# Performance work log

Measured on AMD Instinct MI355X. Metric: run time of the kernel, lower is better.

The kernel has to match this reference:

```python
import jax, jax.numpy as jnp
import numpy as np

HIDDEN = 5120
NUM_HEADS = 32
Q_LORA = 1536
KV_LORA = 512
NOPE = 128
ROPE = 64
V_DIM = 128
QK = NOPE + ROPE  # 192
T = 2048
ROPE_BASE = 10000.0
EPS = 1e-6


def setup_inputs() -> dict:
    key = jax.random.key(0)
    ks = jax.random.split(key, 8)
    s = 0.02
    return {
        "positions": jnp.arange(T, dtype=jnp.int64 if jax.config.jax_enable_x64 else jnp.int32),
        "hidden_states": jax.random.normal(ks[0], (T, HIDDEN), dtype=jnp.float32),
        "w_q_a": jax.random.normal(ks[1], (HIDDEN, Q_LORA), dtype=jnp.float32) * s,
        "q_a_norm": jnp.ones((Q_LORA,), dtype=jnp.float32),
        "w_q_b": jax.random.normal(ks[2], (Q_LORA, NUM_HEADS * QK), dtype=jnp.float32) * s,
        "w_kv_a": jax.random.normal(ks[3], (HIDDEN, KV_LORA + ROPE), dtype=jnp.float32) * s,
        "kv_a_norm": jnp.ones((KV_LORA,), dtype=jnp.float32),
        "w_kv_b": jax.random.normal(ks[4], (KV_LORA, NUM_HEADS * (NOPE + V_DIM)), dtype=jnp.float32) * s,
        "w_o": jax.random.normal(ks[5], (NUM_HEADS * V_DIM, HIDDEN), dtype=jnp.float32) * s,
    }


def _rmsnorm(x, w):
    var = jnp.mean(x * x, axis=-1, keepdims=True)
    return x * jax.lax.rsqrt(var + EPS) * w


def _rope_interleaved(x, positions):
    # x: [T, H, ROPE]; interleaved (GPT-J style) rotation, pairs (x[2i], x[2i+1])
    half = ROPE // 2
    inv_freq = 1.0 / (ROPE_BASE ** (jnp.arange(half, dtype=jnp.float32) * 2.0 / ROPE))
    angles = positions.astype(jnp.float32)[:, None] * inv_freq[None, :]  # [T, half]
    cos = jnp.cos(angles)[:, None, :]  # [T, 1, half]
    sin = jnp.sin(angles)[:, None, :]
    x1 = x[..., 0::2]
    x2 = x[..., 1::2]
    r1 = x1 * cos - x2 * sin
    r2 = x1 * sin + x2 * cos
    return jnp.stack([r1, r2], axis=-1).reshape(x.shape)


def reference(positions, hidden_states, w_q_a, q_a_norm, w_q_b, w_kv_a, kv_a_norm, w_kv_b, w_o):
    # Q path: down-proj -> RMSNorm -> up-proj -> split(nope, rope)
    q_c = _rmsnorm(hidden_states @ w_q_a, q_a_norm)
    q = (q_c @ w_q_b).reshape(T, NUM_HEADS, QK)
    q_nope, q_rope = q[:, :, :NOPE], q[:, :, NOPE:]

    # KV path: joint down-proj -> split(compressed, k_rope) -> RMSNorm -> up-proj
    kv_a = hidden_states @ w_kv_a
    compressed = _rmsnorm(kv_a[:, :KV_LORA], kv_a_norm)
    k_rope_raw = kv_a[:, KV_LORA:].reshape(T, 1, ROPE)
    kv = (compressed @ w_kv_b).reshape(T, NUM_HEADS, NOPE + V_DIM)
    k_nope, v = kv[:, :, :NOPE], kv[:, :, NOPE:]

    # RoPE on rope slices only (interleaved style since rope_interleave=True)
    q_rope = _rope_interleaved(q_rope, positions)
    k_rope = _rope_interleaved(k_rope_raw, positions)
    k_rope = jnp.broadcast_to(k_rope, (T, NUM_HEADS, ROPE))

    q_full = jnp.concatenate([q_nope, q_rope], axis=-1)  # [T, H, QK]
    k_full = jnp.concatenate([k_nope, k_rope], axis=-1)  # [T, H, QK]

    # Causal attention (RadixAttention prefill), scaling = qk_head_dim**-0.5.
    # v is zero-padded to QK in the source and sliced back after; using v
    # directly is mathematically identical.
    scale = QK ** (-0.5)
    scores = jnp.einsum("thd,shd->hts", q_full, k_full) * scale  # [H, T, T]
    causal = positions[:, None] >= positions[None, :]
    scores = jnp.where(causal[None, :, :], scores, jnp.float32(-1e30))
    probs = jax.nn.softmax(scores, axis=-1)
    attn = jnp.einsum("hts,shd->thd", probs, v)  # [T, H, V_DIM]

    out = attn.reshape(T, NUM_HEADS * V_DIM) @ w_o  # [T, HIDDEN]
    return out
```

## Files before the change

### kernel.cpp

```cpp
#include <hip/hip_runtime.h>

typedef unsigned short u16;
typedef unsigned int   u32;
typedef __bf16 bf16x8 __attribute__((ext_vector_type(8)));
typedef float  f32x4  __attribute__((ext_vector_type(4)));
typedef u16    u16x4  __attribute__((ext_vector_type(4)));
typedef u16    u16x8  __attribute__((ext_vector_type(8)));

__device__ __forceinline__ u16 f2bf(float f) {
  u32 u = __float_as_uint(f);
  u32 r = u + 0x7fffu + ((u >> 16) & 1u);
  return (u16)(r >> 16);
}

__device__ __forceinline__ void gl16(const void* g, void* l) {
  __builtin_amdgcn_global_load_lds((__attribute__((address_space(1))) void*)(g),
                                   (__attribute__((address_space(3))) void*)(l),
                                   16, 0, 0);
}

#define WAITVM4  asm volatile("s_waitcnt vmcnt(4)" ::: "memory")
#define WAITVM0  asm volatile("s_waitcnt vmcnt(0)" ::: "memory")
#define WAITLG0  asm volatile("s_waitcnt lgkmcnt(0)" ::: "memory")
#define BAR()    asm volatile("s_barrier" ::: "memory")
#define SCHEDB() __builtin_amdgcn_sched_barrier(0)

__device__ __forceinline__ void tr_tile(const float* __restrict__ W, u16* __restrict__ Wt,
                                        int K, int N, int NT, int idx, float (*tile)[65]) {
  const int tid = threadIdx.x;
  const int nt = idx % NT, kt = idx / NT;
  const int n0 = nt * 64, k0 = kt * 32;
  {
    const int r = tid >> 3, c8 = (tid & 7) << 3;
    const float* src = W + (size_t)(k0 + r) * N + n0 + c8;
    float4 a = *(const float4*)src;
    float4 b = *(const float4*)(src + 4);
    tile[r][c8 + 0] = a.x; tile[r][c8 + 1] = a.y; tile[r][c8 + 2] = a.z; tile[r][c8 + 3] = a.w;
    tile[r][c8 + 4] = b.x; tile[r][c8 + 5] = b.y; tile[r][c8 + 6] = b.z; tile[r][c8 + 7] = b.w;
  }
  __syncthreads();
  const int n = tid >> 2, kg = (tid & 3) << 3;
  u16x8 o;
  #pragma unroll
  for (int j = 0; j < 8; ++j) o[j] = f2bf(tile[kg + j][n]);
  *(u16x8*)(Wt + (size_t)(n0 + n) * K + k0 + kg) = o;
}

__global__ __launch_bounds__(256) void prep_w(const float* __restrict__ hidden, u16* __restrict__ hs_bf,
                                              const float* __restrict__ wqa,  u16* __restrict__ wqa_t,
                                              const float* __restrict__ wkva, u16* __restrict__ wkva_t,
                                              const float* __restrict__ wqb,  u16* __restrict__ wqb_t,
                                              const float* __restrict__ wkvb, u16* __restrict__ wkvb_t,
                                              const float* __restrict__ wo,   u16* __restrict__ wo_t) {
  __shared__ float tile[32][65];
  const int b = blockIdx.x, tid = threadIdx.x;
  if (b < 640) {
    const float4* xin = (const float4*)hidden;
    #pragma unroll
    for (int j = 0; j < 8; ++j) {
      int u = b * 2048 + j * 256 + tid;
      float4 a = xin[u * 2], c = xin[u * 2 + 1];
      u16x8 o;
      o[0] = f2bf(a.x); o[1] = f2bf(a.y); o[2] = f2bf(a.z); o[3] = f2bf(a.w);
      o[4] = f2bf(c.x); o[5] = f2bf(c.y); o[6] = f2bf(c.z); o[7] = f2bf(c.w);
      *(u16x8*)(hs_bf + (size_t)u * 8) = o;
    }
  } else if (b < 4480) {
    tr_tile(wqa, wqa_t, 5120, 1536, 24, b - 640, tile);
  } else if (b < 5920) {
    tr_tile(wkva, wkva_t, 5120, 576, 9, b - 4480, tile);
  } else if (b < 10528) {
    tr_tile(wqb, wqb_t, 1536, 6144, 96, b - 5920, tile);
  } else if (b < 12576) {
    tr_tile(wkvb, wkvb_t, 512, 8192, 128, b - 10528, tile);
  } else if (b < 22816) {
    tr_tile(wo, wo_t, 4096, 5120, 80, b - 12576, tile);
  } else {
    int off = (b - 22816) * 4096 + tid * 16;
    u16x8 z = {};
    *(u16x8*)((char*)wkva_t + (size_t)576 * 5120 * 2 + off) = z;
  }
}

__global__ __launch_bounds__(256) void gemm_a(const u16* __restrict__ A,
                                              const u16* __restrict__ Bt,
                                              float* __restrict__ C,
                                              int M, int N, int K, int nkt) {
  __shared__ u16 As[128 * 64];
  __shared__ u16 Bs[128 * 64];
  const int tid = threadIdx.x;
  const int lane = tid & 63, w = tid >> 6;
  const int n0 = blockIdx.x << 7, m0 = blockIdx.y << 7;
  const int kt0 = blockIdx.z * nkt;
  float* Cs = C + (size_t)blockIdx.z * M * N;
  const int wr = w >> 1, wc = w & 1;
  const int lr = lane & 15, lg = lane >> 4;
  f32x4 acc[4][4] = {};
  const char* Ab = (const char*)A;
  const char* Bb = (const char*)Bt;
  const int stageOff = (w << 10) + (lane << 4);
  for (int kt = 0; kt < nkt; ++kt) {
    __syncthreads();
    const size_t kb = (size_t)(kt0 + kt) << 7;
    #pragma unroll
    for (int o = 0; o < 16384; o += 4096) {
      int ofs = stageOff + o;
      int row = ofs >> 7;
      int cb  = ofs & 127;
      gl16(Ab + (size_t)(m0 + row) * K * 2 + kb + cb, (char*)As + ofs);
      gl16(Bb + (size_t)(n0 + row) * K * 2 + kb + cb, (char*)Bs + ofs);
    }
    __syncthreads();
    bf16x8 a[4][2], b[4][2];
    #pragma unroll
    for (int m = 0; m < 4; ++m)
      #pragma unroll
      for (int kf = 0; kf < 2; ++kf)
        a[m][kf] = *(const bf16x8*)(As + ((wr * 64 + m * 16 + lr) * 64 + kf * 32 + lg * 8));
    #pragma unroll
    for (int n = 0; n < 4; ++n)
      #pragma unroll
      for (int kf = 0; kf < 2; ++kf)
        b[n][kf] = *(const bf16x8*)(Bs + ((wc * 64 + n * 16 + lr) * 64 + kf * 32 + lg * 8));
    #pragma unroll
    for (int kf = 0; kf < 2; ++kf)
      #pragma unroll
      for (int m = 0; m < 4; ++m)
        #pragma unroll
        for (int n = 0; n < 4; ++n)
          acc[m][n] = __builtin_amdgcn_mfma_f32_16x16x32_bf16(a[m][kf], b[n][kf], acc[m][n], 0, 0, 0);
  }
  #pragma unroll
  for (int m = 0; m < 4; ++m) {
    const int row0 = m0 + wr * 64 + m * 16 + lg * 4;
    #pragma unroll
    for (int n = 0; n < 4; ++n) {
      const int col = n0 + wc * 64 + n * 16 + lr;
      #pragma unroll
      for (int r = 0; r < 4; ++r)
        Cs[(size_t)(row0 + r) * N + col] = acc[m][n][r];
    }
  }
}

template<int EPI>
__device__ __forceinline__ void gemm8_body(char* lds,
                                           const u16* __restrict__ A,
                                           const u16* __restrict__ Bt,
                                           int N, int K, int wg, int nwg, int nbx,
                                           const int* __restrict__ pos,
                                           u16* __restrict__ q_all,
                                           u16* __restrict__ k_all,
                                           u16* __restrict__ v_big,
                                           float* __restrict__ Cf) {
  const int nkt = K >> 6;
  const int tid = threadIdx.x;
  const int lane = tid & 63, wid = tid >> 6;
  const int wr = wid >> 2, wc = wid & 3;
  const int lr = lane & 15, lg = lane >> 4;

  const int swz = ((nwg & 7) == 0) ? ((wg & 7) * (nwg >> 3) + (wg >> 3)) : wg;
  const int bx = swz % nbx, by = swz / nbx;
  const int m0 = by << 8, n0 = bx << 8;

  const size_t rs = (size_t)K << 1;
  const char* Ab = (const char*)A;
  const char* Bb = (const char*)Bt;

  const int sofs = tid << 4;
  const int srow = sofs >> 7;
  const int scol = ((((sofs >> 4) & 7) ^ (srow & 7)) << 4);

  const int axor = lr & 7;
  const int sx0 = (lg ^ axor) << 4;
  const int sx1 = ((4 | lg) ^ axor) << 4;
  const int bcolbase = (wc & 1) << 13;

  f32x4 acc[8][4] = {};

#define ASL(p,h) ((((p) << 1) | (h)) << 14)
#define BSL(p,h) (65536 + ((((p) << 1) | (h)) << 14))
#define STAGE_HALF(gb, grow0, kt, slot)                                              \
  { const char* _s = (gb) + (size_t)(grow0) * rs + ((size_t)(kt) << 7) + scol;       \
    gl16(_s, lds + (slot) + sofs);                                                   \
    gl16(_s + (rs << 6), lds + (slot) + sofs + 8192); }

  STAGE_HALF(Ab, m0 + srow,       0, ASL(0,0));
  STAGE_HALF(Ab, m0 + 128 + srow, 0, ASL(0,1));
  STAGE_HALF(Bb, n0 + srow,       0, BSL(0,0));
  STAGE_HALF(Bb, n0 + 128 + srow, 0, BSL(0,1));
  if (nkt > 1) {
    STAGE_HALF(Bb, n0 + srow,       1, BSL(1,0));
    STAGE_HALF(Bb, n0 + 128 + srow, 1, BSL(1,1));
    WAITVM4;
  } else {
    WAITVM0;
  }
  BAR();

  for (int b = 0; b < nkt; ++b) {
    const int p = b & 1;
    const int abase = ASL(p, wr);
    const int bbase = BSL(p, (wc >> 1)) + bcolbase;
    bf16x8 aR[4][2], bR[4][2];

    #pragma unroll
    for (int m = 0; m < 4; ++m) {
      aR[m][0] = *(const bf16x8*)(lds + abase + (m * 16 + lr) * 128 + sx0);
      aR[m][1] = *(const bf16x8*)(lds + abase + (m * 16 + lr) * 128 + sx1);
    }
    #pragma unroll
    for (int n = 0; n < 2; ++n) {
      bR[n][0] = *(const bf16x8*)(lds + bbase + (n * 16 + lr) * 128 + sx0);
      bR[n][1] = *(const bf16x8*)(lds + bbase + (n * 16 + lr) * 128 + sx1);
    }
    if (b + 1 < nkt) { STAGE_HALF(Ab, m0 + srow, b + 1, ASL((b + 1) & 1, 0)); }
    BAR(); WAITLG0; SCHEDB();
    __builtin_amdgcn_s_setprio(1);
    #pragma unroll
    for (int kf = 0; kf < 2; ++kf)
      #pragma unroll
      for (int m = 0; m < 4; ++m)
        #pragma unroll
        for (int n = 0; n < 2; ++n)
          acc[m][n] = __builtin_amdgcn_mfma_f32_16x16x32_bf16(aR[m][kf], bR[n][kf], acc[m][n], 0, 0, 0);
    __builtin_amdgcn_s_setprio(0); SCHEDB();
    BAR();

    #pragma unroll
    for (int n = 2; n < 4; ++n) {
      bR[n][0] = *(const bf16x8*)(lds + bbase + (n * 16 + lr) * 128 + sx0);
      bR[n][1] = *(const bf16x8*)(lds + bbase + (n * 16 + lr) * 128 + sx1);
    }
    if (b + 1 < nkt) { STAGE_HALF(Ab, m0 + 128 + srow, b + 1, ASL((b + 1) & 1, 1)); }
    BAR(); WAITLG0; SCHEDB();
    __builtin_amdgcn_s_setprio(1);
    #pragma unroll
    for (int kf = 0; kf < 2; ++kf)
      #pragma unroll
      for (int m = 0; m < 4; ++m)
        #pragma unroll
        for (int n = 2; n < 4; ++n)
          acc[m][n] = __builtin_amdgcn_mfma_f32_16x16x32_bf16(aR[m][kf], bR[n][kf], acc[m][n], 0, 0, 0);
    __builtin_amdgcn_s_setprio(0); SCHEDB();
    BAR();

    #pragma unroll
    for (int m = 0; m < 4; ++m) {
      aR[m][0] = *(const bf16x8*)(lds + abase + ((m + 4) * 16 + lr) * 128 + sx0);
      aR[m][1] = *(const bf16x8*)(lds + abase + ((m + 4) * 16 + lr) * 128 + sx1);
    }
    if (b + 2 < nkt) { STAGE_HALF(Bb, n0 + srow, b + 2, BSL(p, 0)); }
    BAR(); WAITLG0; SCHEDB();
    __builtin_amdgcn_s_setprio(1);
    #pragma unroll
    for (int kf = 0; kf < 2; ++kf)
      #pragma unroll
      for (int m = 0; m < 4; ++m)
        #pragma unroll
        for (int n = 0; n < 2; ++n)
          acc[m + 4][n] = __builtin_amdgcn_mfma_f32_16x16x32_bf16(aR[m][kf], bR[n][kf], acc[m + 4][n], 0, 0, 0);
    __builtin_amdgcn_s_setprio(0); SCHEDB();
    BAR();

    if (b + 2 < nkt) { STAGE_HALF(Bb, n0 + 128 + srow, b + 2, BSL(p, 1)); }
    BAR(); SCHEDB();
    __builtin_amdgcn_s_setprio(1);
    #pragma unroll
    for (int kf = 0; kf < 2; ++kf)
      #pragma unroll
      for (int m = 0; m < 4; ++m)
        #pragma unroll
        for (int n = 2; n < 4; ++n)
          acc[m + 4][n] = __builtin_amdgcn_mfma_f32_16x16x32_bf16(aR[m][kf], bR[n][kf], acc[m + 4][n], 0, 0, 0);
    __builtin_amdgcn_s_setprio(0); SCHEDB();
    if (b + 2 < nkt) { WAITVM4; } else { WAITVM0; }
    BAR();
  }

  if (EPI == 0) {
    #pragma unroll
    for (int m = 0; m < 8; ++m) {
      const int row0 = m0 + wr * 128 + m * 16 + lg * 4;
      #pragma unroll
      for (int n = 0; n < 4; ++n) {
        const int col = n0 + wc * 64 + n * 16 + lr;
        #pragma unroll
        for (int r = 0; r < 4; ++r)
          Cf[(size_t)(row0 + r) * N + col] = acc[m][n][r];
      }
    }
  } else if (EPI == 1) {
    int hh[4], dd[4]; float inv[4]; bool rope[4];
    #pragma unroll
    for (int n = 0; n < 4; ++n) {
      int col = n0 + wc * 64 + n * 16 + lr;
      hh[n] = col / 192;
      dd[n] = col - hh[n] * 192;
      rope[n] = (dd[n] >= 128);
      int i = (dd[n] - 128) >> 1;
      inv[n] = rope[n] ? exp2f(-(float)i * 0.41524101186092f) : 0.f;
    }
    const bool odd = (lr & 1);
    #pragma unroll
    for (int m = 0; m < 8; ++m) {
      const int row0 = m0 + wr * 128 + m * 16 + lg * 4;
      #pragma unroll
      for (int r = 0; r < 4; ++r) {
        const int row = row0 + r;
        const float pv = (float)pos[row];
        #pragma unroll
        for (int n = 0; n < 4; ++n) {
          float v = acc[m][n][r];
          float o = __shfl_xor(v, 1, 64);
          if (rope[n]) {
            float s, c;
            __sincosf(pv * inv[n], &s, &c);
            v = odd ? (o * s + v * c) : (v * c - o * s);
          }
          q_all[((size_t)hh[n] * 2048 + row) * 192 + dd[n]] = f2bf(v);
        }
      }
    }
  } else {
    #pragma unroll
    for (int m = 0; m < 8; ++m) {
      const int row0 = m0 + wr * 128 + m * 16 + lg * 4;
      #pragma unroll
      for (int r = 0; r < 4; ++r) {
        const int row = row0 + r;
        #pragma unroll
        for (int n = 0; n < 4; ++n) {
          const int col = n0 + wc * 64 + n * 16 + lr;
          const int h = col >> 8, dd = col & 255;
          u16 bv = f2bf(acc[m][n][r]);
          if (dd < 128) k_all[((size_t)h * 2048 + row) * 200 + dd] = bv;
          else          v_big[(size_t)row * 4096 + h * 128 + (dd - 128)] = bv;
        }
      }
    }
  }
#undef ASL
#undef BSL
#undef STAGE_HALF
}

__global__ __launch_bounds__(512, 2) void gemm_fused_b(const u16* __restrict__ A1,
                                                       const u16* __restrict__ B1,
                                                       const u16* __restrict__ A2,
                                                       const u16* __restrict__ B2,
                                                       const int* __restrict__ pos,
                                                       u16* __restrict__ q_all,
                                                       u16* __restrict__ k_all,
                                                       u16* __restrict__ v_big) {
  __shared__ char lds[131072];
  if (blockIdx.x < 192)
    gemm8_body<1>(lds, A1, B1, 6144, 1536, blockIdx.x, 192, 24, pos, q_all, nullptr, nullptr, nullptr);
  else
    gemm8_body<2>(lds, A2, B2, 8192, 512, blockIdx.x - 192, 256, 32, pos, nullptr, k_all, v_big, nullptr);
}

__global__ __launch_bounds__(512, 2) void gemm_out_k(const u16* __restrict__ A,
                                                     const u16* __restrict__ Bt,
                                                     float* __restrict__ C) {
  __shared__ char lds[131072];
  gemm8_body<0>(lds, A, Bt, 5120, 4096, blockIdx.x, 160, 20, nullptr, nullptr, nullptr, nullptr, C);
}

#define SLAB ((size_t)2048 * 2176)
__global__ __launch_bounds__(256) void norm_q_kernel(const float* __restrict__ x,
                                                     const float* __restrict__ w,
                                                     u16* __restrict__ y) {
  const int row = blockIdx.x, tid = threadIdx.x;
  const float* xr = x + (size_t)row * 2176;
  float v[6]; float ss = 0.f;
  #pragma unroll
  for (int i = 0; i < 6; ++i) {
    size_t o = tid + i * 256;
    v[i] = xr[o] + xr[o + SLAB] + xr[o + 2 * SLAB] + xr[o + 3 * SLAB];
    ss += v[i] * v[i];
  }
  __shared__ float sm[4];
  #pragma unroll
  for (int o = 32; o > 0; o >>= 1) ss += __shfl_down(ss, o, 64);
  if ((tid & 63) == 0) sm[tid >> 6] = ss;
  __syncthreads();
  float tot = sm[0] + sm[1] + sm[2] + sm[3];
  float rs = rsqrtf(tot * (1.f / 1536.f) + 1e-6f);
  #pragma unroll
  for (int i = 0; i < 6; ++i)
    y[(size_t)row * 1536 + tid + i * 256] = f2bf(v[i] * rs * w[tid + i * 256]);
}

__global__ __launch_bounds__(256) void norm_kv_kernel(const float* __restrict__ kva,
                                                      const float* __restrict__ w,
                                                      const int* __restrict__ pos,
                                                      u16* __restrict__ comp,
                                                      u16* __restrict__ krope) {
  const int row = blockIdx.x, tid = threadIdx.x;
  const float* xr = kva + (size_t)row * 2176 + 1536;
  float v0 = xr[tid] + xr[tid + SLAB] + xr[tid + 2 * SLAB] + xr[tid + 3 * SLAB];
  size_t o1 = tid + 256;
  float v1 = xr[o1] + xr[o1 + SLAB] + xr[o1 + 2 * SLAB] + xr[o1 + 3 * SLAB];
  float ss = v0 * v0 + v1 * v1;
  __shared__ float sm[4];
  #pragma unroll
  for (int o = 32; o > 0; o >>= 1) ss += __shfl_down(ss, o, 64);
  if ((tid & 63) == 0) sm[tid >> 6] = ss;
  __syncthreads();
  float tot = sm[0] + sm[1] + sm[2] + sm[3];
  float rs = rsqrtf(tot * (1.f / 512.f) + 1e-6f);
  comp[(size_t)row * 512 + tid]       = f2bf(v0 * rs * w[tid]);
  comp[(size_t)row * 512 + tid + 256] = f2bf(v1 * rs * w[tid + 256]);
  if (tid < 32) {
    float p = (float)pos[row];
    float inv = powf(10000.0f, -(float)(2 * tid) * (1.0f / 64.0f));
    float ang = p * inv;
    float c = cosf(ang), s = sinf(ang);
    size_t e1 = 512 + 2 * tid, e2 = e1 + 1;
    float x1 = xr[e1] + xr[e1 + SLAB] + xr[e1 + 2 * SLAB] + xr[e1 + 3 * SLAB];
    float x2 = xr[e2] + xr[e2 + SLAB] + xr[e2 + 2 * SLAB] + xr[e2 + 3 * SLAB];
    krope[(size_t)row * 64 + 2 * tid]     = f2bf(x1 * c - x2 * s);
    krope[(size_t)row * 64 + 2 * tid + 1] = f2bf(x1 * s + x2 * c);
  }
}

__global__ __launch_bounds__(256) void krope_bcast(const u16* __restrict__ krope,
                                                   u16* __restrict__ k_all) {
  const int s = blockIdx.x, tid = threadIdx.x;
  const int h = tid >> 3, j8 = (tid & 7) << 3;
  *(u16x8*)&k_all[((size_t)h * 2048 + s) * 200 + 128 + j8] =
      *(const u16x8*)&krope[(size_t)s * 64 + j8];
}

__global__ __launch_bounds__(256) void v_transpose(const u16* __restrict__ v_big,
                                                   u16* __restrict__ v_t) {
  const int h = blockIdx.x & 31, st = blockIdx.x >> 5, tid = threadIdx.x;
  const int s0 = st * 64;
  __shared__ u16 vs[64][128];
  for (int idx = tid; idx < 4096; idx += 256) {
    int s = idx >> 6, d2 = idx & 63;
    *(u32*)&vs[s][d2 * 2] = *(const u32*)&v_big[(size_t)(s0 + s) * 4096 + h * 128 + d2 * 2];
  }
  __syncthreads();
  const int d = tid >> 1, sh = (tid & 1) * 32;
  u16 tmp[32];
  #pragma unroll
  for (int i = 0; i < 32; ++i) tmp[i] = vs[sh + i][d];
  #pragma unroll
  for (int b = 0; b < 4; ++b) {
    u16x8 o;
    #pragma unroll
    for (int j = 0; j < 8; ++j) o[j] = tmp[b * 8 + j];
    *(u16x8*)(v_t + ((size_t)h * 128 + d) * 2048 + s0 + sh + b * 8) = o;
  }
}

#define SCL2 0.10412706f
#define THR2 11.5f
__global__ __launch_bounds__(512, 2) void attn_fwd(const u16* __restrict__ q_all,
                                                   const u16* __restrict__ k_all,
                                                   const u16* __restrict__ v_t,
                                                   u16* __restrict__ attnb) {
  __shared__ __align__(16) char lds[106496];
  const int tid = threadIdx.x;
  const int lane = tid & 63, wid = tid >> 6;
  const int lr = lane & 15, lg = lane >> 4;
  const int h = blockIdx.x & 31, bq = blockIdx.x >> 5;

  const char* kh = (const char*)(k_all + (size_t)h * 2048 * 200);
  const char* vh = (const char*)(v_t + (size_t)h * 128 * 2048);
  char* Pw = lds + 88064 + wid * 2304;

  const int nCalls = (wid < 3) ? 6 : 5;
  const char* gp[6]; int cofs[6]; int isK[6];
  #pragma unroll
  for (int ii = 0; ii < 6; ++ii) {
    int i = wid + (ii << 3);
    if (i < 43) {
      int c = (i << 6) + lane;
      cofs[ii] = c << 4;
      if (c < 1600) { gp[ii] = kh + ((size_t)c << 4); isK[ii] = 1; }
      else {
        int cv = c - 1600;
        int row = cv / 9, sub = cv - row * 9;
        gp[ii] = vh + ((size_t)row << 12) + ((sub < 8) ? (sub << 4) : 0);
        isK[ii] = 0;
      }
    } else { gp[ii] = kh; cofs[ii] = 0; isK[ii] = 1; }
  }

#define STAGE(s0_, bOff_)                                                       \
  { int _sk = (s0_) * 400, _sv = (s0_) * 2;                                     \
    _Pragma("unroll")                                                           \
    for (int ii = 0; ii < 6; ++ii)                                              \
      if (ii < nCalls)                                                          \
        gl16(gp[ii] + (isK[ii] ? _sk : _sv), lds + (bOff_) + cofs[ii]); }

#define WAITSTAGE                                                               \
  { if (wid < 3) { asm volatile("s_waitcnt vmcnt(6)" ::: "memory"); }           \
    else        { asm volatile("s_waitcnt vmcnt(5)" ::: "memory"); } }

  const int kRd = lr * 400 + lg * 16;
  const int vRd = lr * 144 + lg * 16;
  const int pRd = lr * 144 + lg * 16;
  const int pWr = lr * 144 + lg * 8;

  #pragma unroll
  for (int half = 0; half < 2; ++half) {
    const int qt = half ? (15 - bq) : bq;
    const int qb0 = qt << 7;
    const int nt = 2 * qt + 2;
    const int qlane = qb0 + wid * 16 + lr;
    const int qwmin = qb0 + wid * 16;

    bf16x8 qf[6];
    const u16* qptr = q_all + ((size_t)h * 2048 + qlane) * 192 + lg * 8;
    #pragma unroll
    for (int kf = 0; kf < 6; ++kf) qf[kf] = *(const bf16x8*)(qptr + kf * 32);

    f32x4 O[8] = {};
    float m = -1e30f, l = 0.f;

    STAGE(0, 0);
    for (int st = 0; st < nt; ++st) {
      const int s0 = st << 6;
      const int bOff = (st & 1) * 44032;
      if (st + 1 < nt) {
        STAGE((st + 1) << 6, ((st + 1) & 1) * 44032);
        WAITSTAGE;
      } else {
        WAITVM0;
      }
      BAR();

      const bool active = (s0 <= qwmin + 15);
      if (active) {
        const char* Kb = lds + bOff;
        const char* Vb = lds + bOff + 25600;

        f32x4 S[4];
        #pragma unroll
        for (int sb = 0; sb < 4; ++sb) {
          f32x4 a = {};
          #pragma unroll
          for (int kf = 0; kf < 6; ++kf) {
            bf16x8 kfr = *(const bf16x8*)(Kb + kRd + sb * 6400 + kf * 64);
            a = __builtin_amdgcn_mfma_f32_16x16x32_bf16(kfr, qf[kf], a, 0, 0, 0);
          }
          S[sb] = a;
        }

        if (s0 + 63 > qwmin) {
          const int kb0 = s0 + lg * 4;
          #pragma unroll
          for (int sb = 0; sb < 4; ++sb)
            #pragma unroll
            for (int r = 0; r < 4; ++r) {
              int k = kb0 + sb * 16 + r;
              S[sb][r] = (k > qlane) ? -1e30f : S[sb][r] * SCL2;
            }
        } else {
          #pragma unroll
          for (int sb = 0; sb < 4; ++sb)
            #pragma unroll
            for (int r = 0; r < 4; ++r) S[sb][r] *= SCL2;
        }

        float mx = S[0][0];
        #pragma unroll
        for (int sb = 0; sb < 4; ++sb)
          #pragma unroll
          for (int r = 0; r < 4; ++r) mx = fmaxf(mx, S[sb][r]);
        mx = fmaxf(mx, __shfl_xor(mx, 16, 64));
        mx = fmaxf(mx, __shfl_xor(mx, 32, 64));

        const bool skip = __all(mx <= m + THR2);
        float alpha = 1.f;
        if (!skip) { float mn = fmaxf(m, mx); alpha = exp2f(m - mn); m = mn; }

        float ps = 0.f;
        #pragma unroll
        for (int sb = 0; sb < 4; ++sb)
          #pragma unroll
          for (int r = 0; r < 4; ++r) {
            float pv = exp2f(S[sb][r] - m);
            S[sb][r] = pv;
            ps += pv;
          }
        ps += __shfl_xor(ps, 16, 64);
        ps += __shfl_xor(ps, 32, 64);
        l = l * alpha + ps;

        if (!skip) {
          float aO[4];
          #pragma unroll
          for (int r = 0; r < 4; ++r) aO[r] = __shfl(alpha, lg * 4 + r, 64);
          #pragma unroll
          for (int nb = 0; nb < 8; ++nb)
            #pragma unroll
            for (int r = 0; r < 4; ++r) O[nb][r] *= aO[r];
        }

        #pragma unroll
        for (int sb = 0; sb < 4; ++sb) {
          u32 p01, p23;
          asm("v_cvt_pk_bf16_f32 %0, %1, %2" : "=v"(p01) : "v"(S[sb][0]), "v"(S[sb][1]));
          asm("v_cvt_pk_bf16_f32 %0, %1, %2" : "=v"(p23) : "v"(S[sb][2]), "v"(S[sb][3]));
          *(uint2*)(Pw + pWr + sb * 32) = make_uint2(p01, p23);
        }

        #pragma unroll
        for (int k2 = 0; k2 < 2; ++k2) {
          bf16x8 pa = *(const bf16x8*)(Pw + pRd + k2 * 64);
          #pragma unroll
          for (int nb = 0; nb < 8; ++nb) {
            bf16x8 vf = *(const bf16x8*)(Vb + vRd + nb * 2304 + k2 * 64);
            O[nb] = __builtin_amdgcn_mfma_f32_16x16x32_bf16(pa, vf, O[nb], 0, 0, 0);
          }
        }
      }
      BAR();
    }

    float rv[4];
    #pragma unroll
    for (int r = 0; r < 4; ++r) rv[r] = 1.f / __shfl(l, lg * 4 + r, 64);
    #pragma unroll
    for (int nb = 0; nb < 8; ++nb) {
      const int col = h * 128 + nb * 16 + lr;
      #pragma unroll
      for (int r = 0; r < 4; ++r)
        attnb[(size_t)(qb0 + wid * 16 + lg * 4 + r) * 4096 + col] = f2bf(O[nb][r] * rv[r]);
    }
  }
#undef STAGE
#undef WAITSTAGE
}

extern "C" void kernel_launch(void* const* d_in, const int* in_sizes, int n_in,
                              void* d_out, int out_size, void* d_ws, size_t ws_size,
                              hipStream_t stream) {
  const int*   positions = (const int*)d_in[0];
  const float* hidden    = (const float*)d_in[1];
  const float* w_q_a     = (const float*)d_in[2];
  const float* q_a_norm  = (const float*)d_in[3];
  const float* w_q_b     = (const float*)d_in[4];
  const float* w_kv_a    = (const float*)d_in[5];
  const float* kv_a_norm = (const float*)d_in[6];
  const float* w_kv_b    = (const float*)d_in[7];
  const float* w_o       = (const float*)d_in[8];
  float* out = (float*)d_out;
  char*  ws  = (char*)d_ws;

  u16* hs_bf  = (u16*)(ws + 0);
  u16* attnb  = (u16*)(ws + 0);
  u16* wqa_t  = (u16*)(ws + 20971520);
  u16* wkva_t = (u16*)(ws + 36700160);
  u16* q_c_n  = (u16*)(ws + 20971520);
  u16* comp   = (u16*)(ws + 27262976);
  u16* krope  = (u16*)(ws + 29360128);
  u16* wqb_t  = (u16*)(ws + 43253760);
  u16* wkvb_t = (u16*)(ws + 62128128);
  u16* wo_t   = (u16*)(ws + 70516736);
  float* slabs = (float*)(ws + 112459776);
  u16* q_all  = (u16*)(ws + 112459776);
  u16* k_all  = (u16*)(ws + 137625600);
  u16* v_big  = (u16*)(ws + 183762944);
  u16* v_t    = (u16*)(ws + 200540160);

  prep_w<<<22976, 256, 0, stream>>>(hidden, hs_bf, w_q_a, wqa_t, w_kv_a, wkva_t,
                                    w_q_b, wqb_t, w_kv_b, wkvb_t, w_o, wo_t);

  gemm_a<<<dim3(17, 16, 4), 256, 0, stream>>>(hs_bf, wqa_t, slabs, 2048, 2176, 5120, 20);

  norm_q_kernel<<<2048, 256, 0, stream>>>(slabs, q_a_norm, q_c_n);
  norm_kv_kernel<<<2048, 256, 0, stream>>>(slabs, kv_a_norm, positions, comp, krope);
  krope_bcast<<<2048, 256, 0, stream>>>(krope, k_all);

  gemm_fused_b<<<448, 512, 0, stream>>>(q_c_n, wqb_t, comp, wkvb_t, positions,
                                        q_all, k_all, v_big);

  v_transpose<<<1024, 256, 0, stream>>>(v_big, v_t);

  attn_fwd<<<256, 512, 0, stream>>>(q_all, k_all, v_t, attnb);

  gemm_out_k<<<160, 512, 0, stream>>>(attnb, wo_t, out);
}
```

Before: 453.4 us.

## Replace down-projection GEMM with 256x256 tiled split-K kernel reusing gemm8 body

```diff
diff --git a/kernel.cpp b/kernel.cpp
--- a/kernel.cpp
+++ b/kernel.cpp
@@ -47,8 +47,8 @@
 }
 
 __global__ __launch_bounds__(256) void prep_w(const float* __restrict__ hidden, u16* __restrict__ hs_bf,
-                                              const float* __restrict__ wqa,  u16* __restrict__ wqa_t,
-                                              const float* __restrict__ wkva, u16* __restrict__ wkva_t,
+                                              const float* __restrict__ wqa,
+                                              const float* __restrict__ wkva, u16* __restrict__ wab_t,
                                               const float* __restrict__ wqb,  u16* __restrict__ wqb_t,
                                               const float* __restrict__ wkvb, u16* __restrict__ wkvb_t,
                                               const float* __restrict__ wo,   u16* __restrict__ wo_t) {
@@ -66,9 +66,9 @@
       *(u16x8*)(hs_bf + (size_t)u * 8) = o;
     }
   } else if (b < 4480) {
-    tr_tile(wqa, wqa_t, 5120, 1536, 24, b - 640, tile);
+    tr_tile(wqa, wab_t, 5120, 1536, 24, b - 640, tile);
   } else if (b < 5920) {
-    tr_tile(wkva, wkva_t, 5120, 576, 9, b - 4480, tile);
+    tr_tile(wkva, wab_t + (size_t)1536 * 5120, 5120, 576, 9, b - 4480, tile);
   } else if (b < 10528) {
     tr_tile(wqb, wqb_t, 1536, 6144, 96, b - 5920, tile);
   } else if (b < 12576) {
@@ -76,70 +76,9 @@
   } else if (b < 22816) {
     tr_tile(wo, wo_t, 4096, 5120, 80, b - 12576, tile);
   } else {
-    int off = (b - 22816) * 4096 + tid * 16;
+    size_t off = (size_t)(b - 22816) * 4096 + tid * 16;
     u16x8 z = {};
-    *(u16x8*)((char*)wkva_t + (size_t)576 * 5120 * 2 + off) = z;
-  }
-}
-
-__global__ __launch_bounds__(256) void gemm_a(const u16* __restrict__ A,
-                                              const u16* __restrict__ Bt,
-                                              float* __restrict__ C,
-                                              int M, int N, int K, int nkt) {
-  __shared__ u16 As[128 * 64];
-  __shared__ u16 Bs[128 * 64];
-  const int tid = threadIdx.x;
-  const int lane = tid & 63, w = tid >> 6;
-  const int n0 = blockIdx.x << 7, m0 = blockIdx.y << 7;
-  const int kt0 = blockIdx.z * nkt;
-  float* Cs = C + (size_t)blockIdx.z * M * N;
-  const int wr = w >> 1, wc = w & 1;
-  const int lr = lane & 15, lg = lane >> 4;
-  f32x4 acc[4][4] = {};
-  const char* Ab = (const char*)A;
-  const char* Bb = (const char*)Bt;
-  const int stageOff = (w << 10) + (lane << 4);
-  for (int kt = 0; kt < nkt; ++kt) {
-    __syncthreads();
-    const size_t kb = (size_t)(kt0 + kt) << 7;
-    #pragma unroll
-    for (int o = 0; o < 16384; o += 4096) {
-      int ofs = stageOff + o;
-      int row = ofs >> 7;
-      int cb  = ofs & 127;
-      gl16(Ab + (size_t)(m0 + row) * K * 2 + kb + cb, (char*)As + ofs);
-      gl16(Bb + (size_t)(n0 + row) * K * 2 + kb + cb, (char*)Bs + ofs);
-    }
-    __syncthreads();
-    bf16x8 a[4][2], b[4][2];
-    #pragma unroll
-    for (int m = 0; m < 4; ++m)
-      #pragma unroll
-      for (int kf = 0; kf < 2; ++kf)
-        a[m][kf] = *(const bf16x8*)(As + ((wr * 64 + m * 16 + lr) * 64 + kf * 32 + lg * 8));
-    #pragma unroll
-    for (int n = 0; n < 4; ++n)
-      #pragma unroll
-      for (int kf = 0; kf < 2; ++kf)
-        b[n][kf] = *(const bf16x8*)(Bs + ((wc * 64 + n * 16 + lr) * 64 + kf * 32 + lg * 8));
-    #pragma unroll
-    for (int kf = 0; kf < 2; ++kf)
-      #pragma unroll
-      for (int m = 0; m < 4; ++m)
-        #pragma unroll
-        for (int n = 0; n < 4; ++n)
-          acc[m][n] = __builtin_amdgcn_mfma_f32_16x16x32_bf16(a[m][kf], b[n][kf], acc[m][n], 0, 0, 0);
-  }
-  #pragma unroll
-  for (int m = 0; m < 4; ++m) {
-    const int row0 = m0 + wr * 64 + m * 16 + lg * 4;
-    #pragma unroll
-    for (int n = 0; n < 4; ++n) {
-      const int col = n0 + wc * 64 + n * 16 + lr;
-      #pragma unroll
-      for (int r = 0; r < 4; ++r)
-        Cs[(size_t)(row0 + r) * N + col] = acc[m][n][r];
-    }
+    *(u16x8*)((char*)wab_t + (size_t)2112 * 5120 * 2 + off) = z;
   }
 }
 
@@ -148,12 +87,12 @@
                                            const u16* __restrict__ A,
                                            const u16* __restrict__ Bt,
                                            int N, int K, int wg, int nwg, int nbx,
+                                           int nkt, int kt0,
                                            const int* __restrict__ pos,
                                            u16* __restrict__ q_all,
                                            u16* __restrict__ k_all,
                                            u16* __restrict__ v_big,
                                            float* __restrict__ Cf) {
-  const int nkt = K >> 6;
   const int tid = threadIdx.x;
   const int lane = tid & 63, wid = tid >> 6;
   const int wr = wid >> 2, wc = wid & 3;
@@ -181,7 +120,7 @@
 #define ASL(p,h) ((((p) << 1) | (h)) << 14)
 #define BSL(p,h) (65536 + ((((p) << 1) | (h)) << 14))
 #define STAGE_HALF(gb, grow0, kt, slot)                                              \
-  { const char* _s = (gb) + (size_t)(grow0) * rs + ((size_t)(kt) << 7) + scol;       \
+  { const char* _s = (gb) + (size_t)(grow0) * rs + ((size_t)((kt) + kt0) << 7) + scol; \
     gl16(_s, lds + (slot) + sofs);                                                   \
     gl16(_s + (rs << 6), lds + (slot) + sofs + 8192); }
 
@@ -345,6 +284,19 @@
 #undef STAGE_HALF
 }
 
+#define SLAB2 ((size_t)2048 * 2304)
+__global__ __launch_bounds__(512, 2) void gemm_a8(const u16* __restrict__ A,
+                                                  const u16* __restrict__ Bt,
+                                                  float* __restrict__ C) {
+  __shared__ char lds[131072];
+  const int z = blockIdx.x / 72;
+  const int wg = blockIdx.x - z * 72;
+  const int nkt = (z == 2) ? 26 : 27;
+  const int kt0 = z * 27;
+  gemm8_body<0>(lds, A, Bt, 2304, 5120, wg, 72, 9, nkt, kt0,
+                nullptr, nullptr, nullptr, nullptr, C + (size_t)z * SLAB2);
+}
+
 __global__ __launch_bounds__(512, 2) void gemm_fused_b(const u16* __restrict__ A1,
                                                        const u16* __restrict__ B1,
                                                        const u16* __restrict__ A2,
@@ -355,29 +307,29 @@
                                                        u16* __restrict__ v_big) {
   __shared__ char lds[131072];
   if (blockIdx.x < 192)
-    gemm8_body<1>(lds, A1, B1, 6144, 1536, blockIdx.x, 192, 24, pos, q_all, nullptr, nullptr, nullptr);
+    gemm8_body<1>(lds, A1, B1, 6144, 1536, blockIdx.x, 192, 24, 24, 0, pos, q_all, nullptr, nullptr, nullptr);
   else
-    gemm8_body<2>(lds, A2, B2, 8192, 512, blockIdx.x - 192, 256, 32, pos, nullptr, k_all, v_big, nullptr);
+    gemm8_body<2>(lds, A2, B2, 8192, 512, blockIdx.x - 192, 256, 32, 8, 0, pos, nullptr, k_all, v_big, nullptr);
 }
 
 __global__ __launch_bounds__(512, 2) void gemm_out_k(const u16* __restrict__ A,
                                                      const u16* __restrict__ Bt,
                                                      float* __restrict__ C) {
   __shared__ char lds[131072];
-  gemm8_body<0>(lds, A, Bt, 5120, 4096, blockIdx.x, 160, 20, nullptr, nullptr, nullptr, nullptr, C);
-}
-
-#define SLAB ((size_t)2048 * 2176)
+  gemm8_body<0>(lds, A, Bt, 5120, 4096, blockIdx.x, 160, 20, 64, 0,
+                nullptr, nullptr, nullptr, nullptr, C);
+}
+
 __global__ __launch_bounds__(256) void norm_q_kernel(const float* __restrict__ x,
                                                      const float* __restrict__ w,
                                                      u16* __restrict__ y) {
   const int row = blockIdx.x, tid = threadIdx.x;
-  const float* xr = x + (size_t)row * 2176;
+  const float* xr = x + (size_t)row * 2304;
   float v[6]; float ss = 0.f;
   #pragma unroll
   for (int i = 0; i < 6; ++i) {
     size_t o = tid + i * 256;
-    v[i] = xr[o] + xr[o + SLAB] + xr[o + 2 * SLAB] + xr[o + 3 * SLAB];
+    v[i] = xr[o] + xr[o + SLAB2] + xr[o + 2 * SLAB2];
     ss += v[i] * v[i];
   }
   __shared__ float sm[4];
@@ -398,10 +350,10 @@
                                                       u16* __restrict__ comp,
                                                       u16* __restrict__ krope) {
   const int row = blockIdx.x, tid = threadIdx.x;
-  const float* xr = kva + (size_t)row * 2176 + 1536;
-  float v0 = xr[tid] + xr[tid + SLAB] + xr[tid + 2 * SLAB] + xr[tid + 3 * SLAB];
+  const float* xr = kva + (size_t)row * 2304 + 1536;
+  float v0 = xr[tid] + xr[tid + SLAB2] + xr[tid + 2 * SLAB2];
   size_t o1 = tid + 256;
-  float v1 = xr[o1] + xr[o1 + SLAB] + xr[o1 + 2 * SLAB] + xr[o1 + 3 * SLAB];
+  float v1 = xr[o1] + xr[o1 + SLAB2] + xr[o1 + 2 * SLAB2];
   float ss = v0 * v0 + v1 * v1;
   __shared__ float sm[4];
   #pragma unroll
@@ -418,8 +370,8 @@
     float ang = p * inv;
     float c = cosf(ang), s = sinf(ang);
     size_t e1 = 512 + 2 * tid, e2 = e1 + 1;
-    float x1 = xr[e1] + xr[e1 + SLAB] + xr[e1 + 2 * SLAB] + xr[e1 + 3 * SLAB];
-    float x2 = xr[e2] + xr[e2 + SLAB] + xr[e2 + 2 * SLAB] + xr[e2 + 3 * SLAB];
+    float x1 = xr[e1] + xr[e1 + SLAB2] + xr[e1 + 2 * SLAB2];
+    float x2 = xr[e2] + xr[e2 + SLAB2] + xr[e2 + 2 * SLAB2];
     krope[(size_t)row * 64 + 2 * tid]     = f2bf(x1 * c - x2 * s);
     krope[(size_t)row * 64 + 2 * tid + 1] = f2bf(x1 * s + x2 * c);
   }
@@ -655,24 +607,23 @@
 
   u16* hs_bf  = (u16*)(ws + 0);
   u16* attnb  = (u16*)(ws + 0);
-  u16* wqa_t  = (u16*)(ws + 20971520);
-  u16* wkva_t = (u16*)(ws + 36700160);
+  u16* wab_t  = (u16*)(ws + 20971520);
   u16* q_c_n  = (u16*)(ws + 20971520);
   u16* comp   = (u16*)(ws + 27262976);
   u16* krope  = (u16*)(ws + 29360128);
-  u16* wqb_t  = (u16*)(ws + 43253760);
-  u16* wkvb_t = (u16*)(ws + 62128128);
-  u16* wo_t   = (u16*)(ws + 70516736);
-  float* slabs = (float*)(ws + 112459776);
-  u16* q_all  = (u16*)(ws + 112459776);
-  u16* k_all  = (u16*)(ws + 137625600);
-  u16* v_big  = (u16*)(ws + 183762944);
-  u16* v_t    = (u16*)(ws + 200540160);
-
-  prep_w<<<22976, 256, 0, stream>>>(hidden, hs_bf, w_q_a, wqa_t, w_kv_a, wkva_t,
+  u16* wqb_t  = (u16*)(ws + 44564480);
+  u16* wkvb_t = (u16*)(ws + 63438848);
+  u16* wo_t   = (u16*)(ws + 71827456);
+  float* slabs = (float*)(ws + 113770496);
+  u16* q_all  = (u16*)(ws + 113770496);
+  u16* k_all  = (u16*)(ws + 138936320);
+  u16* v_big  = (u16*)(ws + 170393600);
+  u16* v_t    = (u16*)(ws + 187170816);
+
+  prep_w<<<23296, 256, 0, stream>>>(hidden, hs_bf, w_q_a, w_kv_a, wab_t,
                                     w_q_b, wqb_t, w_kv_b, wkvb_t, w_o, wo_t);
 
-  gemm_a<<<dim3(17, 16, 4), 256, 0, stream>>>(hs_bf, wqa_t, slabs, 2048, 2176, 5120, 20);
+  gemm_a8<<<216, 512, 0, stream>>>(hs_bf, wab_t, slabs);
 
   norm_q_kernel<<<2048, 256, 0, stream>>>(slabs, q_a_norm, q_c_n);
   norm_kv_kernel<<<2048, 256, 0, stream>>>(slabs, kv_a_norm, positions, comp, krope);
```

Measured after the change: 399.3 us. 11.9% less time.
